# Kernel tuning notes

Hardware: AMD Instinct MI355X
Metric: run time of the kernel (lower is better)

Reference implementation:

```python
import jax, jax.numpy as jnp
import numpy as np

N_NODES = 50000
N_EDGES = 600000
N_GRAPHS = 256
IN_C = 128
HID = 128
OUT_C = 2


def setup_inputs() -> dict:
    key = jax.random.key(0)
    ks = jax.random.split(key, 16)
    d = {}
    d["x"] = jax.random.normal(ks[0], (N_NODES, IN_C), jnp.float32)
    d["edge_index"] = jax.random.randint(ks[1], (2, N_EDGES), 0, N_NODES, dtype=jnp.int32)
    d["root_node_idx"] = jax.random.randint(ks[2], (N_GRAPHS,), 0, N_NODES, dtype=jnp.int32)
    d["batch"] = jnp.sort(jax.random.randint(ks[3], (N_NODES,), 0, N_GRAPHS, dtype=jnp.int32))
    dims = [(IN_C, HID), (HID, HID), (HID, HID), (HID, HID)]
    for i, (ci, co) in enumerate(dims, start=1):
        s = 1.0 / np.sqrt(ci)
        d[f"w{i}_l"] = jax.random.uniform(ks[3 + i], (co, ci), jnp.float32, -s, s)
        d[f"b{i}_l"] = jnp.zeros((co,), jnp.float32)
        d[f"w{i}_r"] = jax.random.uniform(ks[7 + i], (co, ci), jnp.float32, -s, s)
    s = 1.0 / np.sqrt(2 * HID)
    d["w_cls"] = jax.random.uniform(ks[12], (OUT_C, 2 * HID), jnp.float32, -s, s)
    d["b_cls"] = jnp.zeros((OUT_C,), jnp.float32)
    return d


def _sage_conv(x, src, tgt, deg_inv, w_l, b_l, w_r):
    # mean aggregation of source features at target nodes (PyG SAGEConv, aggr='mean')
    agg = jax.ops.segment_sum(x[src], tgt, num_segments=N_NODES) * deg_inv  # [N, C]
    # out = lin_l(agg) + lin_r(x); lin_r has no bias in PyG SAGEConv
    return agg @ w_l.T + b_l + x @ w_r.T


def reference(x, edge_index, root_node_idx, batch,
              w1_l, b1_l, w1_r, w2_l, b2_l, w2_r,
              w3_l, b3_l, w3_r, w4_l, b4_l, w4_r,
              w_cls, b_cls):
    src, tgt = edge_index[0], edge_index[1]
    ones_e = jnp.ones((src.shape[0],), x.dtype)
    deg = jax.ops.segment_sum(ones_e, tgt, num_segments=N_NODES)
    deg_inv = (1.0 / jnp.maximum(deg, 1.0))[:, None]  # [N, 1]

    h = jax.nn.relu(_sage_conv(x, src, tgt, deg_inv, w1_l, b1_l, w1_r))
    h = jax.nn.relu(_sage_conv(h, src, tgt, deg_inv, w2_l, b2_l, w2_r))
    h = jax.nn.relu(_sage_conv(h, src, tgt, deg_inv, w3_l, b3_l, w3_r))
    h = jax.nn.relu(_sage_conv(h, src, tgt, deg_inv, w4_l, b4_l, w4_r))

    root_emb = h[root_node_idx]  # [G, HID]
    g_sum = jax.ops.segment_sum(h, batch, num_segments=N_GRAPHS)
    g_cnt = jax.ops.segment_sum(jnp.ones((h.shape[0],), h.dtype), batch, num_segments=N_GRAPHS)
    graph_emb = g_sum / jnp.maximum(g_cnt, 1.0)[:, None]  # [G, HID]

    combined = jnp.concatenate([root_emb, graph_emb], axis=1)  # [G, 2*HID]
    return combined @ w_cls.T + b_cls  # [G, OUT_C]
```

## Files before the change

kernel.cpp:

```cpp
#include <hip/hip_runtime.h>

#define N_NODES 50000
#define N_EDGES 600000
#define N_GRAPHS 256
#define C 128
#define NB 196
#define PB_DEG 2344
#define PB_WS  512

typedef unsigned short ushort;
typedef unsigned int uint;
typedef __attribute__((ext_vector_type(8))) short bfrag8;
typedef __attribute__((ext_vector_type(4))) float facc4;

__device__ __forceinline__ ushort f2bf(float v) {
    uint u = __float_as_uint(v);
    u += 0x7FFFu + ((u >> 16) & 1u);
    return (ushort)(u >> 16);
}
__device__ __forceinline__ float bf2f(ushort u) {
    return __uint_as_float(((uint)u) << 16);
}
__device__ __forceinline__ void fsplit(float v, ushort& h, ushort& l) {
    h = f2bf(v);
    l = f2bf(v - bf2f(h));
}

struct WPtrs { const float* wl[4]; const float* wr[4]; };

__global__ __launch_bounds__(256) void k_prep(const int* __restrict__ tgt,
                                              int* __restrict__ deg,
                                              WPtrs wp,
                                              ushort* __restrict__ BTh,
                                              ushort* __restrict__ BTl,
                                              const int* __restrict__ batch,
                                              int* __restrict__ gstart) {
    const int b = blockIdx.x, t = threadIdx.x;
    if (b < PB_DEG) {
        int e = b * 256 + t;
        if (e < N_EDGES) atomicAdd(&deg[tgt[e]], 1);
    } else if (b < PB_DEG + PB_WS) {
        int gid = (b - PB_DEG) * 256 + t;
        int l = gid >> 15;
        int rem = gid & 32767;
        int n = rem >> 8, k = rem & 255;
        float v = (k < 128) ? wp.wl[l][n * 128 + k] : wp.wr[l][n * 128 + (k - 128)];
        ushort h, lo;
        fsplit(v, h, lo);
        BTh[gid] = h;
        BTl[gid] = lo;
    } else {
        int g = t;
        int lo = 0, hi = N_NODES;
        while (lo < hi) {
            int mid = (lo + hi) >> 1;
            if (batch[mid] < g) lo = mid + 1;
            else hi = mid;
        }
        gstart[g] = lo;
        if (t == 0) gstart[N_GRAPHS] = N_NODES;
    }
}

__global__ __launch_bounds__(256) void k_scan1(const int* __restrict__ deg,
                                               int* __restrict__ bsum,
                                               float* __restrict__ dinv) {
    __shared__ int ws[4];
    int idx = blockIdx.x * 256 + threadIdx.x;
    int v = (idx < N_NODES) ? deg[idx] : 0;
    if (idx < N_NODES) dinv[idx] = 1.0f / fmaxf((float)v, 1.0f);
    int s = v;
#pragma unroll
    for (int off = 1; off < 64; off <<= 1) s += __shfl_xor(s, off);
    if ((threadIdx.x & 63) == 0) ws[threadIdx.x >> 6] = s;
    __syncthreads();
    if (threadIdx.x == 0) bsum[blockIdx.x] = ws[0] + ws[1] + ws[2] + ws[3];
}

__global__ __launch_bounds__(256) void k_scan2(const int* __restrict__ deg,
                                               const int* __restrict__ bsum,
                                               int* __restrict__ rowptr) {
    __shared__ int red[4];
    __shared__ int ws[4];
    const int b = blockIdx.x, t = threadIdx.x;
    const int lane = t & 63, w = t >> 6;
    int bv = (t < NB && t < b) ? bsum[t] : 0;
#pragma unroll
    for (int off = 1; off < 64; off <<= 1) bv += __shfl_xor(bv, off);
    if (lane == 0) red[w] = bv;
    __syncthreads();
    const int boff = red[0] + red[1] + red[2] + red[3];
    int idx = b * 256 + t;
    int v = (idx < N_NODES) ? deg[idx] : 0;
    int incl = v;
#pragma unroll
    for (int off = 1; off < 64; off <<= 1) {
        int u = __shfl_up(incl, off);
        if (lane >= off) incl += u;
    }
    if (lane == 63) ws[w] = incl;
    __syncthreads();
    int wo = 0;
    if (w > 0) wo += ws[0];
    if (w > 1) wo += ws[1];
    if (w > 2) wo += ws[2];
    if (idx < N_NODES) rowptr[idx] = boff + wo + incl - v;
    if (b == 0 && t == 0) rowptr[N_NODES] = N_EDGES;
}

__global__ void k_fill(const int* __restrict__ src, const int* __restrict__ tgt,
                       const int* __restrict__ rowptr, int* __restrict__ fill,
                       int* __restrict__ csr_src) {
    int e = blockIdx.x * blockDim.x + threadIdx.x;
    if (e >= N_EDGES) return;
    int d = tgt[e];
    int pos = atomicAdd(&fill[d], 1);
    csr_src[rowptr[d] + pos] = src[e];
}

__global__ __launch_bounds__(256) void k_gather(const float* __restrict__ Hsrc,
                                                float* __restrict__ AGf,
                                                const int* __restrict__ csr_src,
                                                const int* __restrict__ rowptr,
                                                const float* __restrict__ dinv) {
    int node = blockIdx.x * 8 + (threadIdx.x >> 5);
    if (node >= N_NODES) return;
    int lane = threadIdx.x & 31;
    int c4 = lane << 2;
    int s = rowptr[node], e = rowptr[node + 1];
    float sc = dinv[node];
    float a0 = 0.f, a1 = 0.f, a2 = 0.f, a3 = 0.f;
    int j = s;
    for (; j + 3 < e; j += 4) {
        int s0 = csr_src[j], s1 = csr_src[j + 1];
        int s2 = csr_src[j + 2], s3 = csr_src[j + 3];
        float4 v0 = *(const float4*)(Hsrc + (size_t)s0 * 128 + c4);
        float4 v1 = *(const float4*)(Hsrc + (size_t)s1 * 128 + c4);
        float4 v2 = *(const float4*)(Hsrc + (size_t)s2 * 128 + c4);
        float4 v3 = *(const float4*)(Hsrc + (size_t)s3 * 128 + c4);
        a0 += (v0.x + v1.x) + (v2.x + v3.x);
        a1 += (v0.y + v1.y) + (v2.y + v3.y);
        a2 += (v0.z + v1.z) + (v2.z + v3.z);
        a3 += (v0.w + v1.w) + (v2.w + v3.w);
    }
    for (; j < e; j++) {
        int s0 = csr_src[j];
        float4 v0 = *(const float4*)(Hsrc + (size_t)s0 * 128 + c4);
        a0 += v0.x; a1 += v0.y; a2 += v0.z; a3 += v0.w;
    }
    float4 r; r.x = a0 * sc; r.y = a1 * sc; r.z = a2 * sc; r.w = a3 * sc;
    *(float4*)(AGf + (size_t)node * 128 + c4) = r;
}

__global__ __launch_bounds__(512) void k_gemm(const float* __restrict__ AGf,
                                              const float* __restrict__ Hsrc,
                                              const ushort* __restrict__ BTh,
                                              const ushort* __restrict__ BTl,
                                              const float* __restrict__ bl,
                                              float* __restrict__ Hout) {
    __shared__ short As[2][128][40];
    __shared__ short Bs[2][128][40];
    const int tid = threadIdx.x;
    const int wave = tid >> 6, lane = tid & 63;
    const int m0 = blockIdx.x * 128;
    const int wm = (wave & 1) * 64;
    const int wn = (wave >> 1) * 32;
    const int l15 = lane & 15, lk = (lane >> 4) * 8;

    const int sr = tid >> 2;
    const int sc = (tid & 3) * 8;
    int garow = m0 + sr; if (garow >= N_NODES) garow = N_NODES - 1;
    const float*  pAg = AGf  + (size_t)garow * 128 + sc;
    const float*  pHf = Hsrc + (size_t)garow * 128 + sc;
    const ushort* pBh = BTh + sr * 256 + sc;
    const ushort* pBl = BTl + sr * 256 + sc;

    bfrag8 rBh, rBl;
    float4 f0, f1;
#define LOADSTEP(S) do { \
        const float* pa = ((S) < 4) ? pAg : pHf; \
        f0 = *(const float4*)(pa + ((S) & 3) * 32); \
        f1 = *(const float4*)(pa + ((S) & 3) * 32 + 4); \
        rBh = *(const bfrag8*)(pBh + (S) * 32); \
        rBl = *(const bfrag8*)(pBl + (S) * 32); \
    } while (0)

    LOADSTEP(0);
    facc4 acc[4][2] = {};
#pragma unroll
    for (int s = 0; s < 8; s++) {
        {
            float v[8] = {f0.x, f0.y, f0.z, f0.w, f1.x, f1.y, f1.z, f1.w};
            bfrag8 Hh, Ll;
#pragma unroll
            for (int i = 0; i < 8; i++) {
                ushort hh, ll;
                fsplit(v[i], hh, ll);
                Hh[i] = (short)hh; Ll[i] = (short)ll;
            }
            *(bfrag8*)&As[0][sr][sc] = Hh;
            *(bfrag8*)&As[1][sr][sc] = Ll;
        }
        *(bfrag8*)&Bs[0][sr][sc] = rBh;
        *(bfrag8*)&Bs[1][sr][sc] = rBl;
        __syncthreads();
        if (s < 7) LOADSTEP(s + 1);
        bfrag8 a[2][4], b[2][2];
#pragma unroll
        for (int t = 0; t < 4; t++) {
            a[0][t] = *(const bfrag8*)&As[0][wm + t * 16 + l15][lk];
            a[1][t] = *(const bfrag8*)&As[1][wm + t * 16 + l15][lk];
        }
#pragma unroll
        for (int t = 0; t < 2; t++) {
            b[0][t] = *(const bfrag8*)&Bs[0][wn + t * 16 + l15][lk];
            b[1][t] = *(const bfrag8*)&Bs[1][wn + t * 16 + l15][lk];
        }
#pragma unroll
        for (int mt = 0; mt < 4; mt++)
#pragma unroll
            for (int nt = 0; nt < 2; nt++) {
                acc[mt][nt] = __builtin_amdgcn_mfma_f32_16x16x32_bf16(a[0][mt], b[0][nt], acc[mt][nt], 0, 0, 0);
                acc[mt][nt] = __builtin_amdgcn_mfma_f32_16x16x32_bf16(a[0][mt], b[1][nt], acc[mt][nt], 0, 0, 0);
                acc[mt][nt] = __builtin_amdgcn_mfma_f32_16x16x32_bf16(a[1][mt], b[0][nt], acc[mt][nt], 0, 0, 0);
            }
        __syncthreads();
    }
#undef LOADSTEP

    const int r4 = (lane >> 4) * 4;
#pragma unroll
    for (int mt = 0; mt < 4; mt++) {
#pragma unroll
        for (int nt = 0; nt < 2; nt++) {
            int col = wn + nt * 16 + l15;
            float bias = bl[col];
#pragma unroll
            for (int r = 0; r < 4; r++) {
                int grow = m0 + wm + mt * 16 + r4 + r;
                if (grow < N_NODES) {
                    Hout[(size_t)grow * 128 + col] = fmaxf(acc[mt][nt][r] + bias, 0.f);
                }
            }
        }
    }
}

__global__ __launch_bounds__(256) void k_head(const float* __restrict__ H,
                                              const int* __restrict__ gstart,
                                              const int* __restrict__ root,
                                              const float* __restrict__ wcls,
                                              const float* __restrict__ bcls,
                                              float* __restrict__ out) {
    __shared__ float gm[128];
    __shared__ float part[128];
    __shared__ float red[8];
    const int g = blockIdx.x, t = threadIdx.x;
    const int c = t & 127, p = t >> 7;
    int s = gstart[g], e = gstart[g + 1];
    float sum = 0.f;
    for (int n = s + p; n < e; n += 2) {
        sum += H[(size_t)n * 128 + c];
    }
    if (p) part[c] = sum;
    __syncthreads();
    if (!p) gm[c] = (sum + part[c]) / fmaxf((float)(e - s), 1.0f);
    __syncthreads();
    float v;
    if (t < 128) {
        v = H[(size_t)root[g] * 128 + t];
    } else {
        v = gm[t - 128];
    }
    float p0 = v * wcls[t];
    float p1 = v * wcls[256 + t];
#pragma unroll
    for (int off = 32; off; off >>= 1) {
        p0 += __shfl_down(p0, off);
        p1 += __shfl_down(p1, off);
    }
    int wid = t >> 6;
    if ((t & 63) == 0) { red[wid] = p0; red[4 + wid] = p1; }
    __syncthreads();
    if (t == 0) {
        out[g * 2 + 0] = red[0] + red[1] + red[2] + red[3] + bcls[0];
        out[g * 2 + 1] = red[4] + red[5] + red[6] + red[7] + bcls[1];
    }
}

extern "C" void kernel_launch(void* const* d_in, const int* in_sizes, int n_in,
                              void* d_out, int out_size, void* d_ws, size_t ws_size,
                              hipStream_t stream) {
    const float* x = (const float*)d_in[0];
    const int* ei = (const int*)d_in[1];
    const int* src = ei;
    const int* tgt = ei + N_EDGES;
    const int* root = (const int*)d_in[2];
    const int* batch = (const int*)d_in[3];
    WPtrs wp;
    wp.wl[0] = (const float*)d_in[4];  wp.wr[0] = (const float*)d_in[6];
    wp.wl[1] = (const float*)d_in[7];  wp.wr[1] = (const float*)d_in[9];
    wp.wl[2] = (const float*)d_in[10]; wp.wr[2] = (const float*)d_in[12];
    wp.wl[3] = (const float*)d_in[13]; wp.wr[3] = (const float*)d_in[15];
    const float* blv[4] = {(const float*)d_in[5], (const float*)d_in[8],
                           (const float*)d_in[11], (const float*)d_in[14]};
    const float* wcls = (const float*)d_in[16];
    const float* bcls = (const float*)d_in[17];
    float* out = (float*)d_out;

    float* H = (float*)d_ws;
    float* AGf = H + (size_t)N_NODES * 128;
    ushort* BTh = (ushort*)(AGf + (size_t)N_NODES * 128);
    ushort* BTl = BTh + 4 * 128 * 256;
    int* deg = (int*)(BTl + 4 * 128 * 256);
    int* fill = deg + N_NODES;
    float* dinv = (float*)(fill + N_NODES);
    int* rowptr = (int*)(dinv + N_NODES);
    int* csr_src = rowptr + N_NODES + 1;
    int* bsum = csr_src + N_EDGES;
    int* gstart = bsum + 256;

    hipMemsetAsync(deg, 0, 2 * N_NODES * sizeof(int), stream);
    k_prep<<<PB_DEG + PB_WS + 1, 256, 0, stream>>>(
        tgt, deg, wp, BTh, BTl, batch, gstart);
    k_scan1<<<NB, 256, 0, stream>>>(deg, bsum, dinv);
    k_scan2<<<NB, 256, 0, stream>>>(deg, bsum, rowptr);
    k_fill<<<(N_EDGES + 255) / 256, 256, 0, stream>>>(src, tgt, rowptr, fill, csr_src);

    for (int l = 0; l < 4; l++) {
        const float* hsrc = (l == 0) ? x : H;
        k_gather<<<(N_NODES + 7) / 8, 256, 0, stream>>>(hsrc, AGf, csr_src, rowptr, dinv);
        k_gemm<<<(N_NODES + 127) / 128, 512, 0, stream>>>(
            AGf, hsrc, BTh + l * 32768, BTl + l * 32768, blv[l], H);
    }
    k_head<<<N_GRAPHS, 256, 0, stream>>>(H, gstart, root, wcls, bcls, out);
}
```

Before: 446.0 us.

## Fuse neighbor mean-aggregation into GEMM kernel via shared-memory aggregate tile

Merges the separate gather and GEMM kernels into one kernel per layer. Each 64-node block first aggregates neighbor features into shared memory, then feeds that tile to the split-bf16 MFMA GEMM alongside the self features. This removes the AGf round trip through global memory and one launch per layer. Layers now ping-pong between two H buffers because a block reads other nodes' rows while writing its own. The price is a smaller M tile per block with B reloaded more often, plus larger shared memory per block (~54KB) that may cut occupancy during the latency-bound gather phase.

```diff
diff --git a/kernel.cpp b/kernel.cpp
--- a/kernel.cpp
+++ b/kernel.cpp
@@ -118,71 +118,78 @@
     csr_src[rowptr[d] + pos] = src[e];
 }
 
-__global__ __launch_bounds__(256) void k_gather(const float* __restrict__ Hsrc,
-                                                float* __restrict__ AGf,
-                                                const int* __restrict__ csr_src,
-                                                const int* __restrict__ rowptr,
-                                                const float* __restrict__ dinv) {
-    int node = blockIdx.x * 8 + (threadIdx.x >> 5);
-    if (node >= N_NODES) return;
-    int lane = threadIdx.x & 31;
-    int c4 = lane << 2;
-    int s = rowptr[node], e = rowptr[node + 1];
-    float sc = dinv[node];
-    float a0 = 0.f, a1 = 0.f, a2 = 0.f, a3 = 0.f;
-    int j = s;
-    for (; j + 3 < e; j += 4) {
-        int s0 = csr_src[j], s1 = csr_src[j + 1];
-        int s2 = csr_src[j + 2], s3 = csr_src[j + 3];
-        float4 v0 = *(const float4*)(Hsrc + (size_t)s0 * 128 + c4);
-        float4 v1 = *(const float4*)(Hsrc + (size_t)s1 * 128 + c4);
-        float4 v2 = *(const float4*)(Hsrc + (size_t)s2 * 128 + c4);
-        float4 v3 = *(const float4*)(Hsrc + (size_t)s3 * 128 + c4);
-        a0 += (v0.x + v1.x) + (v2.x + v3.x);
-        a1 += (v0.y + v1.y) + (v2.y + v3.y);
-        a2 += (v0.z + v1.z) + (v2.z + v3.z);
-        a3 += (v0.w + v1.w) + (v2.w + v3.w);
-    }
-    for (; j < e; j++) {
-        int s0 = csr_src[j];
-        float4 v0 = *(const float4*)(Hsrc + (size_t)s0 * 128 + c4);
-        a0 += v0.x; a1 += v0.y; a2 += v0.z; a3 += v0.w;
-    }
-    float4 r; r.x = a0 * sc; r.y = a1 * sc; r.z = a2 * sc; r.w = a3 * sc;
-    *(float4*)(AGf + (size_t)node * 128 + c4) = r;
-}
-
-__global__ __launch_bounds__(512) void k_gemm(const float* __restrict__ AGf,
-                                              const float* __restrict__ Hsrc,
-                                              const ushort* __restrict__ BTh,
-                                              const ushort* __restrict__ BTl,
-                                              const float* __restrict__ bl,
-                                              float* __restrict__ Hout) {
-    __shared__ short As[2][128][40];
+__global__ __launch_bounds__(256) void k_fused(const float* __restrict__ Hsrc,
+                                               const ushort* __restrict__ BTh,
+                                               const ushort* __restrict__ BTl,
+                                               const float* __restrict__ bl,
+                                               float* __restrict__ Hout,
+                                               const int* __restrict__ csr_src,
+                                               const int* __restrict__ rowptr,
+                                               const float* __restrict__ dinv) {
+    __shared__ float agg[64][132];
+    __shared__ short As[2][64][40];
     __shared__ short Bs[2][128][40];
     const int tid = threadIdx.x;
+    const int m0 = blockIdx.x * 64;
+
+    {
+        const int g = tid >> 5;
+        const int lane32 = tid & 31;
+        const int c4 = lane32 << 2;
+        for (int ni = g; ni < 64; ni += 8) {
+            int node = m0 + ni;
+            if (node >= N_NODES) break;
+            int s = rowptr[node], e = rowptr[node + 1];
+            float sc = dinv[node];
+            float a0 = 0.f, a1 = 0.f, a2 = 0.f, a3 = 0.f;
+            int j = s;
+            for (; j + 3 < e; j += 4) {
+                int s0 = csr_src[j], s1 = csr_src[j + 1];
+                int s2 = csr_src[j + 2], s3 = csr_src[j + 3];
+                float4 v0 = *(const float4*)(Hsrc + (size_t)s0 * 128 + c4);
+                float4 v1 = *(const float4*)(Hsrc + (size_t)s1 * 128 + c4);
+                float4 v2 = *(const float4*)(Hsrc + (size_t)s2 * 128 + c4);
+                float4 v3 = *(const float4*)(Hsrc + (size_t)s3 * 128 + c4);
+                a0 += (v0.x + v1.x) + (v2.x + v3.x);
+                a1 += (v0.y + v1.y) + (v2.y + v3.y);
+                a2 += (v0.z + v1.z) + (v2.z + v3.z);
+                a3 += (v0.w + v1.w) + (v2.w + v3.w);
+            }
+            for (; j < e; j++) {
+                int s0 = csr_src[j];
+                float4 v0 = *(const float4*)(Hsrc + (size_t)s0 * 128 + c4);
+                a0 += v0.x; a1 += v0.y; a2 += v0.z; a3 += v0.w;
+            }
+            float4 r; r.x = a0 * sc; r.y = a1 * sc; r.z = a2 * sc; r.w = a3 * sc;
+            *(float4*)&agg[ni][c4] = r;
+        }
+    }
+    __syncthreads();
+
     const int wave = tid >> 6, lane = tid & 63;
-    const int m0 = blockIdx.x * 128;
-    const int wm = (wave & 1) * 64;
-    const int wn = (wave >> 1) * 32;
+    const int wn = wave * 32;
     const int l15 = lane & 15, lk = (lane >> 4) * 8;
 
-    const int sr = tid >> 2;
-    const int sc = (tid & 3) * 8;
-    int garow = m0 + sr; if (garow >= N_NODES) garow = N_NODES - 1;
-    const float*  pAg = AGf  + (size_t)garow * 128 + sc;
-    const float*  pHf = Hsrc + (size_t)garow * 128 + sc;
-    const ushort* pBh = BTh + sr * 256 + sc;
-    const ushort* pBl = BTl + sr * 256 + sc;
-
-    bfrag8 rBh, rBl;
+    const int sr4 = tid >> 2;
+    const int sc4 = (tid & 3) * 8;
+    const int sr2 = tid >> 1;
+    const int sc2 = (tid & 1) * 16;
+    int garow = m0 + sr4; if (garow >= N_NODES) garow = N_NODES - 1;
+    const float*  pHf = Hsrc + (size_t)garow * 128 + sc4;
+    const ushort* pBh = BTh + sr2 * 256 + sc2;
+    const ushort* pBl = BTl + sr2 * 256 + sc2;
+
+    bfrag8 rBh0, rBh1, rBl0, rBl1;
     float4 f0, f1;
 #define LOADSTEP(S) do { \
-        const float* pa = ((S) < 4) ? pAg : pHf; \
-        f0 = *(const float4*)(pa + ((S) & 3) * 32); \
-        f1 = *(const float4*)(pa + ((S) & 3) * 32 + 4); \
-        rBh = *(const bfrag8*)(pBh + (S) * 32); \
-        rBl = *(const bfrag8*)(pBl + (S) * 32); \
+        if ((S) >= 4) { \
+            f0 = *(const float4*)(pHf + ((S) & 3) * 32); \
+            f1 = *(const float4*)(pHf + ((S) & 3) * 32 + 4); \
+        } \
+        rBh0 = *(const bfrag8*)(pBh + (S) * 32); \
+        rBh1 = *(const bfrag8*)(pBh + (S) * 32 + 8); \
+        rBl0 = *(const bfrag8*)(pBl + (S) * 32); \
+        rBl1 = *(const bfrag8*)(pBl + (S) * 32 + 8); \
     } while (0)
 
     LOADSTEP(0);
@@ -190,7 +197,16 @@
 #pragma unroll
     for (int s = 0; s < 8; s++) {
         {
-            float v[8] = {f0.x, f0.y, f0.z, f0.w, f1.x, f1.y, f1.z, f1.w};
+            float v[8];
+            if (s < 4) {
+                float4 g0 = *(const float4*)&agg[sr4][s * 32 + sc4];
+                float4 g1 = *(const float4*)&agg[sr4][s * 32 + sc4 + 4];
+                v[0] = g0.x; v[1] = g0.y; v[2] = g0.z; v[3] = g0.w;
+                v[4] = g1.x; v[5] = g1.y; v[6] = g1.z; v[7] = g1.w;
+            } else {
+                v[0] = f0.x; v[1] = f0.y; v[2] = f0.z; v[3] = f0.w;
+                v[4] = f1.x; v[5] = f1.y; v[6] = f1.z; v[7] = f1.w;
+            }
             bfrag8 Hh, Ll;
 #pragma unroll
             for (int i = 0; i < 8; i++) {
@@ -198,18 +214,20 @@
                 fsplit(v[i], hh, ll);
                 Hh[i] = (short)hh; Ll[i] = (short)ll;
             }
-            *(bfrag8*)&As[0][sr][sc] = Hh;
-            *(bfrag8*)&As[1][sr][sc] = Ll;
-        }
-        *(bfrag8*)&Bs[0][sr][sc] = rBh;
-        *(bfrag8*)&Bs[1][sr][sc] = rBl;
+            *(bfrag8*)&As[0][sr4][sc4] = Hh;
+            *(bfrag8*)&As[1][sr4][sc4] = Ll;
+        }
+        *(bfrag8*)&Bs[0][sr2][sc2]     = rBh0;
+        *(bfrag8*)&Bs[0][sr2][sc2 + 8] = rBh1;
+        *(bfrag8*)&Bs[1][sr2][sc2]     = rBl0;
+        *(bfrag8*)&Bs[1][sr2][sc2 + 8] = rBl1;
         __syncthreads();
         if (s < 7) LOADSTEP(s + 1);
         bfrag8 a[2][4], b[2][2];
 #pragma unroll
         for (int t = 0; t < 4; t++) {
-            a[0][t] = *(const bfrag8*)&As[0][wm + t * 16 + l15][lk];
-            a[1][t] = *(const bfrag8*)&As[1][wm + t * 16 + l15][lk];
+            a[0][t] = *(const bfrag8*)&As[0][t * 16 + l15][lk];
+            a[1][t] = *(const bfrag8*)&As[1][t * 16 + l15][lk];
         }
 #pragma unroll
         for (int t = 0; t < 2; t++) {
@@ -237,7 +255,7 @@
             float bias = bl[col];
 #pragma unroll
             for (int r = 0; r < 4; r++) {
-                int grow = m0 + wm + mt * 16 + r4 + r;
+                int grow = m0 + mt * 16 + r4 + r;
                 if (grow < N_NODES) {
                     Hout[(size_t)grow * 128 + col] = fmaxf(acc[mt][nt][r] + bias, 0.f);
                 }
@@ -308,9 +326,9 @@
     const float* bcls = (const float*)d_in[17];
     float* out = (float*)d_out;
 
-    float* H = (float*)d_ws;
-    float* AGf = H + (size_t)N_NODES * 128;
-    ushort* BTh = (ushort*)(AGf + (size_t)N_NODES * 128);
+    float* HA = (float*)d_ws;
+    float* HB = HA + (size_t)N_NODES * 128;
+    ushort* BTh = (ushort*)(HB + (size_t)N_NODES * 128);
     ushort* BTl = BTh + 4 * 128 * 256;
     int* deg = (int*)(BTl + 4 * 128 * 256);
     int* fill = deg + N_NODES;
@@ -327,11 +345,12 @@
     k_scan2<<<NB, 256, 0, stream>>>(deg, bsum, rowptr);
     k_fill<<<(N_EDGES + 255) / 256, 256, 0, stream>>>(src, tgt, rowptr, fill, csr_src);
 
+    const float* srcs[4] = {x, HA, HB, HA};
+    float* dsts[4]       = {HA, HB, HA, HB};
+    const int FB = (N_NODES + 63) / 64;
     for (int l = 0; l < 4; l++) {
-        const float* hsrc = (l == 0) ? x : H;
-        k_gather<<<(N_NODES + 7) / 8, 256, 0, stream>>>(hsrc, AGf, csr_src, rowptr, dinv);
-        k_gemm<<<(N_NODES + 127) / 128, 512, 0, stream>>>(
-            AGf, hsrc, BTh + l * 32768, BTl + l * 32768, blv[l], H);
-    }
-    k_head<<<N_GRAPHS, 256, 0, stream>>>(H, gstart, root, wcls, bcls, out);
-}
+        k_fused<<<FB, 256, 0, stream>>>(srcs[l], BTh + l * 32768, BTl + l * 32768,
+                                        blv[l], dsts[l], csr_src, rowptr, dinv);
+    }
+    k_head<<<N_GRAPHS, 256, 0, stream>>>(HB, gstart, root, wcls, bcls, out);
+}
```

Result: slower. 602.1 us (+35.0%).

## Fuse graph-build kernels into one cooperative kernel with grid syncs

Applied to the files above, without the earlier changes.

Replaces the memset, prep, two scan kernels and the CSR fill kernel with a single cooperative launch of 1024 blocks that separates the phases with grid-wide syncs. Zeroing of the degree and fill arrays moves into the kernel. The aim is to remove several launch gaps and the memset from the preprocessing chain. In exchange it adds grid.sync barriers, limits the edge loops to a fixed grid with strided iteration, and requires the cooperative launch to fit 1024 resident blocks.

```diff
diff --git a/kernel.cpp b/kernel.cpp
--- a/kernel.cpp
+++ b/kernel.cpp
@@ -1,12 +1,15 @@
 #include <hip/hip_runtime.h>
+#include <hip/hip_cooperative_groups.h>
+
+namespace cg = cooperative_groups;
 
 #define N_NODES 50000
 #define N_EDGES 600000
 #define N_GRAPHS 256
 #define C 128
 #define NB 196
-#define PB_DEG 2344
-#define PB_WS  512
+#define BUILD_BLOCKS 1024
+#define BUILD_THREADS (BUILD_BLOCKS * 256)
 
 typedef unsigned short ushort;
 typedef unsigned int uint;
@@ -28,19 +31,29 @@
 
 struct WPtrs { const float* wl[4]; const float* wr[4]; };
 
-__global__ __launch_bounds__(256) void k_prep(const int* __restrict__ tgt,
-                                              int* __restrict__ deg,
-                                              WPtrs wp,
-                                              ushort* __restrict__ BTh,
-                                              ushort* __restrict__ BTl,
-                                              const int* __restrict__ batch,
-                                              int* __restrict__ gstart) {
+__global__ __launch_bounds__(256, 4) void k_build(const int* __restrict__ src,
+                                                  const int* __restrict__ tgt,
+                                                  int* __restrict__ deg,
+                                                  WPtrs wp,
+                                                  ushort* __restrict__ BTh,
+                                                  ushort* __restrict__ BTl,
+                                                  const int* __restrict__ batch,
+                                                  int* __restrict__ gstart,
+                                                  float* __restrict__ dinv,
+                                                  int* __restrict__ rowptr,
+                                                  int* __restrict__ csr_src,
+                                                  int* __restrict__ bsum) {
+    cg::grid_group grid = cg::this_grid();
+    __shared__ int ws[4];
+    __shared__ int red[4];
     const int b = blockIdx.x, t = threadIdx.x;
-    if (b < PB_DEG) {
-        int e = b * 256 + t;
-        if (e < N_EDGES) atomicAdd(&deg[tgt[e]], 1);
-    } else if (b < PB_DEG + PB_WS) {
-        int gid = (b - PB_DEG) * 256 + t;
+    const int gtid = b * 256 + t;
+    int* fill = deg + N_NODES;
+
+    if (gtid < 2 * N_NODES) {
+        deg[gtid] = 0;
+    } else if (gtid < 2 * N_NODES + 131072) {
+        int gid = gtid - 2 * N_NODES;
         int l = gid >> 15;
         int rem = gid & 32767;
         int n = rem >> 8, k = rem & 255;
@@ -49,8 +62,8 @@
         fsplit(v, h, lo);
         BTh[gid] = h;
         BTl[gid] = lo;
-    } else {
-        int g = t;
+    } else if (gtid < 2 * N_NODES + 131072 + 256) {
+        int g = gtid - (2 * N_NODES + 131072);
         int lo = 0, hi = N_NODES;
         while (lo < hi) {
             int mid = (lo + hi) >> 1;
@@ -58,64 +71,60 @@
             else hi = mid;
         }
         gstart[g] = lo;
-        if (t == 0) gstart[N_GRAPHS] = N_NODES;
-    }
-}
-
-__global__ __launch_bounds__(256) void k_scan1(const int* __restrict__ deg,
-                                               int* __restrict__ bsum,
-                                               float* __restrict__ dinv) {
-    __shared__ int ws[4];
-    int idx = blockIdx.x * 256 + threadIdx.x;
-    int v = (idx < N_NODES) ? deg[idx] : 0;
-    if (idx < N_NODES) dinv[idx] = 1.0f / fmaxf((float)v, 1.0f);
-    int s = v;
-#pragma unroll
-    for (int off = 1; off < 64; off <<= 1) s += __shfl_xor(s, off);
-    if ((threadIdx.x & 63) == 0) ws[threadIdx.x >> 6] = s;
-    __syncthreads();
-    if (threadIdx.x == 0) bsum[blockIdx.x] = ws[0] + ws[1] + ws[2] + ws[3];
-}
-
-__global__ __launch_bounds__(256) void k_scan2(const int* __restrict__ deg,
-                                               const int* __restrict__ bsum,
-                                               int* __restrict__ rowptr) {
-    __shared__ int red[4];
-    __shared__ int ws[4];
-    const int b = blockIdx.x, t = threadIdx.x;
-    const int lane = t & 63, w = t >> 6;
-    int bv = (t < NB && t < b) ? bsum[t] : 0;
-#pragma unroll
-    for (int off = 1; off < 64; off <<= 1) bv += __shfl_xor(bv, off);
-    if (lane == 0) red[w] = bv;
-    __syncthreads();
-    const int boff = red[0] + red[1] + red[2] + red[3];
-    int idx = b * 256 + t;
-    int v = (idx < N_NODES) ? deg[idx] : 0;
-    int incl = v;
-#pragma unroll
-    for (int off = 1; off < 64; off <<= 1) {
-        int u = __shfl_up(incl, off);
-        if (lane >= off) incl += u;
-    }
-    if (lane == 63) ws[w] = incl;
-    __syncthreads();
-    int wo = 0;
-    if (w > 0) wo += ws[0];
-    if (w > 1) wo += ws[1];
-    if (w > 2) wo += ws[2];
-    if (idx < N_NODES) rowptr[idx] = boff + wo + incl - v;
-    if (b == 0 && t == 0) rowptr[N_NODES] = N_EDGES;
-}
-
-__global__ void k_fill(const int* __restrict__ src, const int* __restrict__ tgt,
-                       const int* __restrict__ rowptr, int* __restrict__ fill,
-                       int* __restrict__ csr_src) {
-    int e = blockIdx.x * blockDim.x + threadIdx.x;
-    if (e >= N_EDGES) return;
-    int d = tgt[e];
-    int pos = atomicAdd(&fill[d], 1);
-    csr_src[rowptr[d] + pos] = src[e];
+        if (g == 0) gstart[N_GRAPHS] = N_NODES;
+    }
+    grid.sync();
+
+    for (int e = gtid; e < N_EDGES; e += BUILD_THREADS) {
+        atomicAdd(&deg[tgt[e]], 1);
+    }
+    grid.sync();
+
+    if (b < NB) {
+        int idx = b * 256 + t;
+        int v = (idx < N_NODES) ? deg[idx] : 0;
+        if (idx < N_NODES) dinv[idx] = 1.0f / fmaxf((float)v, 1.0f);
+        int s = v;
+#pragma unroll
+        for (int off = 1; off < 64; off <<= 1) s += __shfl_xor(s, off);
+        if ((t & 63) == 0) ws[t >> 6] = s;
+        __syncthreads();
+        if (t == 0) bsum[b] = ws[0] + ws[1] + ws[2] + ws[3];
+    }
+    grid.sync();
+
+    if (b < NB) {
+        const int lane = t & 63, w = t >> 6;
+        int bv = (t < NB && t < b) ? bsum[t] : 0;
+#pragma unroll
+        for (int off = 1; off < 64; off <<= 1) bv += __shfl_xor(bv, off);
+        if (lane == 0) red[w] = bv;
+        __syncthreads();
+        const int boff = red[0] + red[1] + red[2] + red[3];
+        int idx = b * 256 + t;
+        int v = (idx < N_NODES) ? deg[idx] : 0;
+        int incl = v;
+#pragma unroll
+        for (int off = 1; off < 64; off <<= 1) {
+            int u = __shfl_up(incl, off);
+            if (lane >= off) incl += u;
+        }
+        if (lane == 63) ws[w] = incl;
+        __syncthreads();
+        int wo = 0;
+        if (w > 0) wo += ws[0];
+        if (w > 1) wo += ws[1];
+        if (w > 2) wo += ws[2];
+        if (idx < N_NODES) rowptr[idx] = boff + wo + incl - v;
+        if (b == 0 && t == 0) rowptr[N_NODES] = N_EDGES;
+    }
+    grid.sync();
+
+    for (int e = gtid; e < N_EDGES; e += BUILD_THREADS) {
+        int d = tgt[e];
+        int pos = atomicAdd(&fill[d], 1);
+        csr_src[rowptr[d] + pos] = src[e];
+    }
 }
 
 __global__ __launch_bounds__(256) void k_gather(const float* __restrict__ Hsrc,
@@ -319,13 +328,15 @@
     int* csr_src = rowptr + N_NODES + 1;
     int* bsum = csr_src + N_EDGES;
     int* gstart = bsum + 256;
-
-    hipMemsetAsync(deg, 0, 2 * N_NODES * sizeof(int), stream);
-    k_prep<<<PB_DEG + PB_WS + 1, 256, 0, stream>>>(
-        tgt, deg, wp, BTh, BTl, batch, gstart);
-    k_scan1<<<NB, 256, 0, stream>>>(deg, bsum, dinv);
-    k_scan2<<<NB, 256, 0, stream>>>(deg, bsum, rowptr);
-    k_fill<<<(N_EDGES + 255) / 256, 256, 0, stream>>>(src, tgt, rowptr, fill, csr_src);
+    (void)fill;
+
+    {
+        void* args[] = {(void*)&src, (void*)&tgt, (void*)&deg, (void*)&wp,
+                        (void*)&BTh, (void*)&BTl, (void*)&batch, (void*)&gstart,
+                        (void*)&dinv, (void*)&rowptr, (void*)&csr_src, (void*)&bsum};
+        hipLaunchCooperativeKernel((void*)k_build, dim3(BUILD_BLOCKS), dim3(256),
+                                   args, 0, stream);
+    }
 
     for (int l = 0; l < 4; l++) {
         const float* hsrc = (l == 0) ? x : H;
```

Result: slower. 856.6 us (+92.1%).
